# Optimization experiments

Hardware: AMD Instinct MI355X
Metric: run time of the kernel (lower is better)

Reference implementation:

```python
import jax, jax.numpy as jnp
import numpy as np

P = 8.0  # Lp exponent of the distance neuron (finite-p stage of l_inf-dist training)


def _patches(t, k, stride, pad):
    # [B, Cin, H, W] -> [B, Cin*k*k, H', W'], feature dim ordered channel-major
    return jax.lax.conv_general_dilated_patches(
        t, (k, k), (stride, stride), [(pad, pad), (pad, pad)])


def _lp(d):
    # d: [B, Cout, Cin*k*k, H', W'] nonnegative -> Lp norm over patch dim
    return jnp.power(jnp.sum(jnp.power(d, P), axis=2), 1.0 / P)


def norm_dist_conv(x, l, u, w, stride, pad):
    # Lp-distance "convolution": y[b,o,i,j] = || patch(x)[b,:,i,j] - w[o,:] ||_p
    # mean_normalize=True: zero-center each output unit's weight vector
    Cout, Cin, k, _ = w.shape
    wf = w.reshape(Cout, -1)
    wf = wf - jnp.mean(wf, axis=1, keepdims=True)
    wb = wf[None, :, :, None, None]                      # [1, Cout, Ckk, 1, 1]
    px = _patches(x, k, stride, pad)[:, None]            # [B, 1, Ckk, H', W']
    pl = _patches(l, k, stride, pad)[:, None]
    pu = _patches(u, k, stride, pad)[:, None]
    y = _lp(jnp.abs(px - wb))
    # interval bounds of |x_j - w_j| given x_j in [l_j, u_j], then monotone Lp
    dl = jnp.maximum(jnp.maximum(pl - wb, wb - pu), 0.0)
    du = jnp.maximum(jnp.abs(pl - wb), jnp.abs(pu - wb))
    return y, _lp(dl), _lp(du)


def bound_relu(x, l, u):
    # ReLU is monotone: apply elementwise to value and both bounds
    return jax.nn.relu(x), jax.nn.relu(l), jax.nn.relu(u)


def setup_inputs() -> dict:
    key = jax.random.key(0)
    k1, k2, k3 = jax.random.split(key, 3)
    B, C, H, W = 4, 32, 32, 32
    eps = 0.1  # l_inf perturbation radius
    x = jax.random.normal(k1, (B, C, H, W), dtype=jnp.float32)
    lower = x - eps
    upper = x + eps
    scale = 1.0 / np.sqrt(C * 9)
    weight1 = jax.random.normal(k2, (C, C, 3, 3), dtype=jnp.float32) * scale
    weight2 = jax.random.normal(k3, (C, C, 3, 3), dtype=jnp.float32) * scale
    return {"x": x, "lower": lower, "upper": upper,
            "weight1": weight1, "weight2": weight2}


def reference(x, lower, upper, weight1, weight2):
    # conv1 (stride=1, pad=1) -> BoundReLU -> conv2 -> residual add -> BoundReLU
    o = norm_dist_conv(x, lower, upper, weight1, 1, 1)
    o = bound_relu(*o)
    o = norm_dist_conv(*o, weight2, 1, 1)
    out = (o[0] + x, o[1] + lower, o[2] + upper)  # identity shortcut (stride=1, in==out)
    out = bound_relu(*out)
    return jnp.stack(out)  # [3, B, C, H, W]: (value, lower, upper)
```

## Files before the change

### kernel.cpp

```cpp
#include <hip/hip_runtime.h>

#define NB 4
#define NC 32
#define NH 32
#define NW 32
#define KK 288
#define PLANE (NB*NC*NH*NW)
#define CHALF 16

__device__ __forceinline__ float s3(float v) { return sqrtf(sqrtf(sqrtf(v))); }

__global__ __launch_bounds__(256) void prep_weights_k(
        const float* __restrict__ w1, const float* __restrict__ w2,
        float* __restrict__ wf1, float* __restrict__ wf2)
{
    const int row = blockIdx.x;
    const float* src = (row < NC) ? w1 : w2;
    float* dst = (row < NC) ? wf1 : wf2;
    const int co = row & (NC - 1);
    const int tid = threadIdx.x;
    __shared__ float red[256];
    const float a = src[co*KK + tid];
    const float b = (tid + 256 < KK) ? src[co*KK + tid + 256] : 0.0f;
    red[tid] = a + b;
    __syncthreads();
    for (int s = 128; s > 0; s >>= 1) {
        if (tid < s) red[tid] += red[tid + s];
        __syncthreads();
    }
    const float mean = red[0] * (1.0f / (float)KK);
    {
        const int e = tid, c = e / 9, r9 = e - c*9, r = r9 / 3, kw = r9 - r*3;
        dst[co*384 + ((c*3 + r) << 2) + kw] = a - mean;
    }
    if (tid + 256 < KK) {
        const int e = tid + 256, c = e / 9, r9 = e - c*9, r = r9 / 3, kw = r9 - r*3;
        dst[co*384 + ((c*3 + r) << 2) + kw] = b - mean;
    }
}

template<bool STAGE2>
__global__ __launch_bounds__(256, 4) void normdist_conv_k(
    const float* __restrict__ sy,
    const float* __restrict__ sl,
    const float* __restrict__ su,
    const float* __restrict__ wf,
    float* __restrict__ pY, float* __restrict__ pL, float* __restrict__ pU)
{
    const int h     = blockIdx.x;
    const int cog   = blockIdx.y >> 1;
    const int chalf = blockIdx.y & 1;
    const int ch0   = chalf * CHALF;
    const int b     = blockIdx.z;
    const int tx    = threadIdx.x;
    const int ty    = threadIdx.y;
    const int tid   = ty * 32 + tx;

    __shared__ float4 sP[CHALF*3*34];

    for (int i = tid; i < CHALF*3*34; i += 256) {
        const int c   = i / 102;
        const int rem = i - c*102;
        const int r   = rem / 34;
        const int col = rem - r*34;
        const int gh  = h + r - 1;
        const int gw  = col - 1;
        float vx = 0.0f, vl = 0.0f, vu = 0.0f;
        if ((unsigned)gh < NH && (unsigned)gw < NW) {
            const int g = ((b*NC + ch0 + c)*NH + gh)*NW + gw;
            if (STAGE2) {
                vx = s3(sy[g] + sy[PLANE + g]);
                vl = s3(sl[g] + sl[PLANE + g]);
                vu = s3(su[g] + su[PLANE + g]);
            } else {
                vx = sy[g]; vl = sl[g]; vu = su[g];
            }
        }
        sP[i] = make_float4(vx, vl, vu, 0.0f);
    }
    __syncthreads();

    const int co = cog*8 + ty;
    const float4* wbase = (const float4*)wf + (co*NC + ch0)*3;

    float accY = 0.0f, accL = 0.0f, accU = 0.0f;

    auto tap = [&](float wv, float4 p) {
        const float d  = p.x - wv;
        const float d2 = d*d, d4 = d2*d2;
        accY = fmaf(d4, d4, accY);
        const float a  = p.y - wv;
        const float nb = wv - p.z;
        const float m  = fmaxf(fmaxf(a, nb), 0.0f);
        const float m2 = m*m, m4 = m2*m2;
        accL = fmaf(m4, m4, accL);
        const float a2 = a*a, q2 = nb*nb;
        const float mm2 = fmaxf(a2, q2);
        const float mm4 = mm2*mm2;
        accU = fmaf(mm4, mm4, accU);
    };

    #pragma unroll 2
    for (int c = 0; c < CHALF; ++c) {
        const float4 w0 = wbase[c*3 + 0];
        const float4 w1 = wbase[c*3 + 1];
        const float4 w2 = wbase[c*3 + 2];
        const int pb = c*102 + tx;
        tap(w0.x, sP[pb +  0]); tap(w0.y, sP[pb +  1]); tap(w0.z, sP[pb +  2]);
        tap(w1.x, sP[pb + 34]); tap(w1.y, sP[pb + 35]); tap(w1.z, sP[pb + 36]);
        tap(w2.x, sP[pb + 68]); tap(w2.y, sP[pb + 69]); tap(w2.z, sP[pb + 70]);
    }

    const int o = ((b*NC + co)*NH + h)*NW + tx;
    pY[chalf*PLANE + o] = accY;
    pL[chalf*PLANE + o] = accL;
    pU[chalf*PLANE + o] = accU;
}

__global__ __launch_bounds__(256) void epilogue_k(
    const float* __restrict__ pY, const float* __restrict__ pL, const float* __restrict__ pU,
    const float* __restrict__ x,  const float* __restrict__ l,  const float* __restrict__ u,
    float* __restrict__ out)
{
    const int o = blockIdx.x*256 + threadIdx.x;
    const float y  = s3(pY[o] + pY[PLANE + o]);
    const float dl = s3(pL[o] + pL[PLANE + o]);
    const float du = s3(pU[o] + pU[PLANE + o]);
    out[o]           = fmaxf(y  + x[o], 0.0f);
    out[PLANE + o]   = fmaxf(dl + l[o], 0.0f);
    out[2*PLANE + o] = fmaxf(du + u[o], 0.0f);
}

extern "C" void kernel_launch(void* const* d_in, const int* in_sizes, int n_in,
                              void* d_out, int out_size, void* d_ws, size_t ws_size,
                              hipStream_t stream)
{
    const float* x  = (const float*)d_in[0];
    const float* l  = (const float*)d_in[1];
    const float* u  = (const float*)d_in[2];
    const float* w1 = (const float*)d_in[3];
    const float* w2 = (const float*)d_in[4];
    float* ws  = (float*)d_ws;
    float* wf1 = ws;
    float* wf2 = wf1 + 12288;
    float* p1Y = wf2 + 12288;
    float* p1L = p1Y + 2*PLANE;
    float* p1U = p1L + 2*PLANE;
    float* p2Y = p1U + 2*PLANE;
    float* p2L = p2Y + 2*PLANE;
    float* p2U = p2L + 2*PLANE;
    float* out = (float*)d_out;

    prep_weights_k<<<64, 256, 0, stream>>>(w1, w2, wf1, wf2);

    dim3 blk(32, 8);
    dim3 grd(NH, 8, NB);
    normdist_conv_k<false><<<grd, blk, 0, stream>>>(x, l, u, wf1, p1Y, p1L, p1U);
    normdist_conv_k<true ><<<grd, blk, 0, stream>>>(p1Y, p1L, p1U, wf2, p2Y, p2L, p2U);
    epilogue_k<<<PLANE/256, 256, 0, stream>>>(p2Y, p2L, p2U, x, l, u, out);
}
```

Baseline: 107.6 us.

## Split input channels into quarters and compute two output channels per thread

The channel reduction is split four ways instead of two, so each block holds 8 input channels in shared memory. Each thread now computes two output channels (co and co+8) and reuses the same loaded patch values for both, which halves shared-memory reads per tap. The grid size stays the same, but the partial-sum buffers double and the stage-2 loader and epilogue must sum four partials. That adds global traffic and uses more registers per thread. The upper-bound term also switches to a fabs-max form, which saves one multiply per tap.

```diff
diff --git a/kernel.cpp b/kernel.cpp
--- a/kernel.cpp
+++ b/kernel.cpp
@@ -6,7 +6,7 @@
 #define NW 32
 #define KK 288
 #define PLANE (NB*NC*NH*NW)
-#define CHALF 16
+#define CQ 8
 
 __device__ __forceinline__ float s3(float v) { return sqrtf(sqrtf(sqrtf(v))); }
 
@@ -47,18 +47,18 @@
     const float* __restrict__ wf,
     float* __restrict__ pY, float* __restrict__ pL, float* __restrict__ pU)
 {
-    const int h     = blockIdx.x;
-    const int cog   = blockIdx.y >> 1;
-    const int chalf = blockIdx.y & 1;
-    const int ch0   = chalf * CHALF;
-    const int b     = blockIdx.z;
-    const int tx    = threadIdx.x;
-    const int ty    = threadIdx.y;
-    const int tid   = ty * 32 + tx;
+    const int h   = blockIdx.x;
+    const int cog = blockIdx.y >> 2;
+    const int q   = blockIdx.y & 3;
+    const int ch0 = q * CQ;
+    const int b   = blockIdx.z;
+    const int tx  = threadIdx.x;
+    const int ty  = threadIdx.y;
+    const int tid = ty * 32 + tx;
 
-    __shared__ float4 sP[CHALF*3*34];
+    __shared__ float4 sP[CQ*3*34];
 
-    for (int i = tid; i < CHALF*3*34; i += 256) {
+    for (int i = tid; i < CQ*3*34; i += 256) {
         const int c   = i / 102;
         const int rem = i - c*102;
         const int r   = rem / 34;
@@ -69,9 +69,9 @@
         if ((unsigned)gh < NH && (unsigned)gw < NW) {
             const int g = ((b*NC + ch0 + c)*NH + gh)*NW + gw;
             if (STAGE2) {
-                vx = s3(sy[g] + sy[PLANE + g]);
-                vl = s3(sl[g] + sl[PLANE + g]);
-                vu = s3(su[g] + su[PLANE + g]);
+                vx = s3(sy[g] + sy[PLANE + g] + sy[2*PLANE + g] + sy[3*PLANE + g]);
+                vl = s3(sl[g] + sl[PLANE + g] + sl[2*PLANE + g] + sl[3*PLANE + g]);
+                vu = s3(su[g] + su[PLANE + g] + su[2*PLANE + g] + su[3*PLANE + g]);
             } else {
                 vx = sy[g]; vl = sl[g]; vu = su[g];
             }
@@ -80,41 +80,48 @@
     }
     __syncthreads();
 
-    const int co = cog*8 + ty;
-    const float4* wbase = (const float4*)wf + (co*NC + ch0)*3;
+    const int co0 = cog*16 + ty;
+    const int co1 = co0 + 8;
+    const float4* wb0 = (const float4*)wf + (co0*NC + ch0)*3;
+    const float4* wb1 = (const float4*)wf + (co1*NC + ch0)*3;
 
-    float accY = 0.0f, accL = 0.0f, accU = 0.0f;
+    float y0 = 0.0f, l0 = 0.0f, u0 = 0.0f;
+    float y1 = 0.0f, l1 = 0.0f, u1 = 0.0f;
 
-    auto tap = [&](float wv, float4 p) {
+    auto tap = [](float wv, float4 p, float& aY, float& aL, float& aU) {
         const float d  = p.x - wv;
         const float d2 = d*d, d4 = d2*d2;
-        accY = fmaf(d4, d4, accY);
+        aY = fmaf(d4, d4, aY);
         const float a  = p.y - wv;
         const float nb = wv - p.z;
         const float m  = fmaxf(fmaxf(a, nb), 0.0f);
         const float m2 = m*m, m4 = m2*m2;
-        accL = fmaf(m4, m4, accL);
-        const float a2 = a*a, q2 = nb*nb;
-        const float mm2 = fmaxf(a2, q2);
-        const float mm4 = mm2*mm2;
-        accU = fmaf(mm4, mm4, accU);
+        aL = fmaf(m4, m4, aL);
+        const float mm  = fmaxf(fabsf(a), fabsf(nb));
+        const float mm2 = mm*mm, mm4 = mm2*mm2;
+        aU = fmaf(mm4, mm4, aU);
     };
 
     #pragma unroll 2
-    for (int c = 0; c < CHALF; ++c) {
-        const float4 w0 = wbase[c*3 + 0];
-        const float4 w1 = wbase[c*3 + 1];
-        const float4 w2 = wbase[c*3 + 2];
+    for (int c = 0; c < CQ; ++c) {
+        const float4 wA0 = wb0[c*3 + 0], wA1 = wb0[c*3 + 1], wA2 = wb0[c*3 + 2];
+        const float4 wB0 = wb1[c*3 + 0], wB1 = wb1[c*3 + 1], wB2 = wb1[c*3 + 2];
         const int pb = c*102 + tx;
-        tap(w0.x, sP[pb +  0]); tap(w0.y, sP[pb +  1]); tap(w0.z, sP[pb +  2]);
-        tap(w1.x, sP[pb + 34]); tap(w1.y, sP[pb + 35]); tap(w1.z, sP[pb + 36]);
-        tap(w2.x, sP[pb + 68]); tap(w2.y, sP[pb + 69]); tap(w2.z, sP[pb + 70]);
+        const float4 p00 = sP[pb +  0], p01 = sP[pb +  1], p02 = sP[pb +  2];
+        const float4 p10 = sP[pb + 34], p11 = sP[pb + 35], p12 = sP[pb + 36];
+        const float4 p20 = sP[pb + 68], p21 = sP[pb + 69], p22 = sP[pb + 70];
+        tap(wA0.x, p00, y0,l0,u0); tap(wA0.y, p01, y0,l0,u0); tap(wA0.z, p02, y0,l0,u0);
+        tap(wA1.x, p10, y0,l0,u0); tap(wA1.y, p11, y0,l0,u0); tap(wA1.z, p12, y0,l0,u0);
+        tap(wA2.x, p20, y0,l0,u0); tap(wA2.y, p21, y0,l0,u0); tap(wA2.z, p22, y0,l0,u0);
+        tap(wB0.x, p00, y1,l1,u1); tap(wB0.y, p01, y1,l1,u1); tap(wB0.z, p02, y1,l1,u1);
+        tap(wB1.x, p10, y1,l1,u1); tap(wB1.y, p11, y1,l1,u1); tap(wB1.z, p12, y1,l1,u1);
+        tap(wB2.x, p20, y1,l1,u1); tap(wB2.y, p21, y1,l1,u1); tap(wB2.z, p22, y1,l1,u1);
     }
 
-    const int o = ((b*NC + co)*NH + h)*NW + tx;
-    pY[chalf*PLANE + o] = accY;
-    pL[chalf*PLANE + o] = accL;
-    pU[chalf*PLANE + o] = accU;
+    const int o0 = ((b*NC + co0)*NH + h)*NW + tx;
+    const int o1 = ((b*NC + co1)*NH + h)*NW + tx;
+    pY[q*PLANE + o0] = y0;  pL[q*PLANE + o0] = l0;  pU[q*PLANE + o0] = u0;
+    pY[q*PLANE + o1] = y1;  pL[q*PLANE + o1] = l1;  pU[q*PLANE + o1] = u1;
 }
 
 __global__ __launch_bounds__(256) void epilogue_k(
@@ -123,9 +130,9 @@
     float* __restrict__ out)
 {
     const int o = blockIdx.x*256 + threadIdx.x;
-    const float y  = s3(pY[o] + pY[PLANE + o]);
-    const float dl = s3(pL[o] + pL[PLANE + o]);
-    const float du = s3(pU[o] + pU[PLANE + o]);
+    const float y  = s3(pY[o] + pY[PLANE + o] + pY[2*PLANE + o] + pY[3*PLANE + o]);
+    const float dl = s3(pL[o] + pL[PLANE + o] + pL[2*PLANE + o] + pL[3*PLANE + o]);
+    const float du = s3(pU[o] + pU[PLANE + o] + pU[2*PLANE + o] + pU[3*PLANE + o]);
     out[o]           = fmaxf(y  + x[o], 0.0f);
     out[PLANE + o]   = fmaxf(dl + l[o], 0.0f);
     out[2*PLANE + o] = fmaxf(du + u[o], 0.0f);
@@ -144,11 +151,11 @@
     float* wf1 = ws;
     float* wf2 = wf1 + 12288;
     float* p1Y = wf2 + 12288;
-    float* p1L = p1Y + 2*PLANE;
-    float* p1U = p1L + 2*PLANE;
-    float* p2Y = p1U + 2*PLANE;
-    float* p2L = p2Y + 2*PLANE;
-    float* p2U = p2L + 2*PLANE;
+    float* p1L = p1Y + 4*PLANE;
+    float* p1U = p1L + 4*PLANE;
+    float* p2Y = p1U + 4*PLANE;
+    float* p2L = p2Y + 4*PLANE;
+    float* p2U = p2L + 4*PLANE;
     float* out = (float*)d_out;
 
     prep_weights_k<<<64, 256, 0, stream>>>(w1, w2, wf1, wf2);
```

Measured after the change: 116.8 us. 8.6% more time.
